# Kernel optimization log

Measured on AMD Instinct MI355X. Metric: run time of the kernel, lower is better.

## Reference

```python
import jax, jax.numpy as jnp
import numpy as np

H = 8        # n_attention_heads
D = 512      # model_dimension (full per-head dim in this module!)
DFF = 2048   # feed_forward_internal_dimension
B, T = 8, 1024
EPS = 1e-5


def _layernorm(x, g, b, eps=EPS):
    mu = jnp.mean(x, axis=-1, keepdims=True)
    var = jnp.mean(jnp.square(x - mu), axis=-1, keepdims=True)
    return (x - mu) * jax.lax.rsqrt(var + eps) * g + b


def setup_inputs() -> dict:
    key = jax.random.key(0)
    ks = jax.random.split(key, 16)
    s_d = 1.0 / np.sqrt(D)
    s_c = 1.0 / np.sqrt(H * D)
    s_f = 1.0 / np.sqrt(DFF)
    return {
        "x":   jax.random.normal(ks[0], (B, T, D), jnp.float32),
        # per-head projections, stored (in, out); stacked over heads
        "Wq":  jax.random.normal(ks[1], (H, D, D), jnp.float32) * s_d,
        "bq":  jax.random.normal(ks[2], (H, D), jnp.float32) * 0.02,
        "Wk":  jax.random.normal(ks[3], (H, D, D), jnp.float32) * s_d,
        "bk":  jax.random.normal(ks[4], (H, D), jnp.float32) * 0.02,
        "Wv":  jax.random.normal(ks[5], (H, D, D), jnp.float32) * s_d,
        "bv":  jax.random.normal(ks[6], (H, D), jnp.float32) * 0.02,
        "Wo":  jax.random.normal(ks[7], (H * D, D), jnp.float32) * s_c,
        "bo":  jax.random.normal(ks[8], (D,), jnp.float32) * 0.02,
        "ln1_g": 1.0 + 0.1 * jax.random.normal(ks[9], (D,), jnp.float32),
        "ln1_b": 0.1 * jax.random.normal(ks[10], (D,), jnp.float32),
        "W1":  jax.random.normal(ks[11], (D, DFF), jnp.float32) * s_d,
        "b1":  jax.random.normal(ks[12], (DFF,), jnp.float32) * 0.02,
        "W2":  jax.random.normal(ks[13], (DFF, D), jnp.float32) * s_f,
        "b2":  jax.random.normal(ks[14], (D,), jnp.float32) * 0.02,
        "ln2_g": 1.0 + 0.1 * jax.random.normal(ks[15], (D,), jnp.float32),
        "ln2_b": jnp.zeros((D,), jnp.float32),
    }


def reference(x, Wq, bq, Wk, bk, Wv, bv, Wo, bo, ln1_g, ln1_b,
              W1, b1, W2, b2, ln2_g, ln2_b):
    # --- multi-head attention (each head uses the FULL d_model) ---
    # q,k,v: [H, B, T, D]
    q = jnp.einsum("btd,hde->hbte", x, Wq) + bq[:, None, None, :]
    k = jnp.einsum("btd,hde->hbte", x, Wk) + bk[:, None, None, :]
    v = jnp.einsum("btd,hde->hbte", x, Wv) + bv[:, None, None, :]
    scores = jnp.einsum("hbte,hbse->hbts", q, k) * (D ** -0.5)  # [H,B,T,T]
    attn = jax.nn.softmax(scores, axis=-1)
    heads = jnp.einsum("hbts,hbse->hbte", attn, v)  # [H,B,T,D]
    # concat heads along features: [B,T,H*D]
    concat = jnp.transpose(heads, (1, 2, 0, 3)).reshape(x.shape[0], x.shape[1], -1)
    mha = concat @ Wo + bo
    # residual + LayerNorm (dropout_p = 0)
    y1 = _layernorm(mha + x, ln1_g, ln1_b)
    # --- FFN: note source applies ReLU AFTER the second Linear, then skip ---
    ff = jax.nn.relu((y1 @ W1 + b1) @ W2 + b2) + y1
    out = _layernorm(ff, ln2_g, ln2_b)
    return out
```

## Files before the change

kernel.cpp:

```cpp
#include <hip/hip_runtime.h>

using u16 = unsigned short;
using bf16x8 = __attribute__((ext_vector_type(8))) short;
using f32x4 = __attribute__((ext_vector_type(4))) float;
using f32x16 = __attribute__((ext_vector_type(16))) float;

__device__ __forceinline__ u16 f2bf(float f) {
  unsigned x = __float_as_uint(f);
  x += 0x7fffu + ((x >> 16) & 1u);
  return (u16)(x >> 16);
}

__device__ __forceinline__ void gl2lds16(const u16* g, u16* l) {
  __builtin_amdgcn_global_load_lds(
      (const __attribute__((address_space(1))) unsigned int*)g,
      (__attribute__((address_space(3))) unsigned int*)l, 16, 0, 0);
}

__global__ __launch_bounds__(256) void cvt_all(
    const float* __restrict__ x, u16* __restrict__ Krep,
    const float* __restrict__ Wq, const float* __restrict__ Wk,
    const float* __restrict__ Wv, const float* __restrict__ Wo,
    const float* __restrict__ W1, const float* __restrict__ W2,
    u16* __restrict__ Wqb, u16* __restrict__ Wkb, u16* __restrict__ WvT,
    u16* __restrict__ WoT, u16* __restrict__ W1T, u16* __restrict__ W2T)
{
  int b = blockIdx.x, tid = threadIdx.x;
  if (b < 4096) {
    int i = b * 1024 + tid * 4;
    float4 v = *(const float4*)(x + i);
    ushort4 o;
    o.x = f2bf(v.x); o.y = f2bf(v.y); o.z = f2bf(v.z); o.w = f2bf(v.w);
    *(ushort4*)(Krep + i) = o;
    return;
  }
  if (b < 8192) {
    const float* s; u16* d; int i;
    if (b < 6144) { s = Wq; d = Wqb; i = (b - 4096) * 1024 + tid * 4; }
    else          { s = Wk; d = Wkb; i = (b - 6144) * 1024 + tid * 4; }
    float4 v = *(const float4*)(s + i);
    ushort4 o;
    o.x = f2bf(v.x); o.y = f2bf(v.y); o.z = f2bf(v.z); o.w = f2bf(v.w);
    *(ushort4*)(d + i) = o;
    return;
  }
  __shared__ float T[32][33];
  const float* s; u16* d; int K, N, k0, n0;
  int i = b - 8192;
  if (i < 2048) {
    int h = i / 256, tl = i % 256;
    s = Wv + (size_t)h * 262144; d = WvT + (size_t)h * 262144;
    K = 512; N = 512; n0 = (tl % 16) * 32; k0 = (tl / 16) * 32;
  } else if (i < 4096) {
    int j = i - 2048;
    s = Wo; d = WoT; K = 4096; N = 512; n0 = (j % 16) * 32; k0 = (j / 16) * 32;
  } else if (i < 5120) {
    int j = i - 4096;
    s = W1; d = W1T; K = 512; N = 2048; n0 = (j % 64) * 32; k0 = (j / 64) * 32;
  } else {
    int j = i - 5120;
    s = W2; d = W2T; K = 2048; N = 512; n0 = (j % 16) * 32; k0 = (j / 16) * 32;
  }
  int r = tid >> 3, c4 = (tid & 7) << 2;
  float4 v = *(const float4*)(s + (size_t)(k0 + r) * N + n0 + c4);
  T[r][c4 + 0] = v.x; T[r][c4 + 1] = v.y; T[r][c4 + 2] = v.z; T[r][c4 + 3] = v.w;
  __syncthreads();
  ushort4 o;
  o.x = f2bf(T[c4 + 0][r]); o.y = f2bf(T[c4 + 1][r]);
  o.z = f2bf(T[c4 + 2][r]); o.w = f2bf(T[c4 + 3][r]);
  *(ushort4*)(d + (size_t)(n0 + r) * K + k0 + c4) = o;
}

__global__ __launch_bounds__(256) void wk_bias(
    const float* __restrict__ Wk, const float* __restrict__ bq,
    float* __restrict__ wbuf)
{
  int r = blockIdx.x * 4 + (threadIdx.x >> 6);
  int lane = threadIdx.x & 63;
  int h = r >> 9, a = r & 511;
  const float* row = Wk + ((size_t)h * 512 + a) * 512 + lane * 8;
  const float* bqp = bq + h * 512 + lane * 8;
  float4 w0 = *(const float4*)row, w1 = *(const float4*)(row + 4);
  float4 b0 = *(const float4*)bqp, b1 = *(const float4*)(bqp + 4);
  float s = w0.x * b0.x + w0.y * b0.y + w0.z * b0.z + w0.w * b0.w +
            w1.x * b1.x + w1.y * b1.y + w1.z * b1.z + w1.w * b1.w;
  #pragma unroll
  for (int off = 1; off < 64; off <<= 1) s += __shfl_xor(s, off);
  if (lane == 0) wbuf[r] = s;
}

template<int BM>
__global__ __launch_bounds__(256) void gemm_bt(
    const u16* __restrict__ A, const u16* __restrict__ Bt,
    const float* __restrict__ bias, void* __restrict__ Cout,
    int M, int N, int K, int lda, int ldb, long long kzoff,
    long long sBz, long long sbz, long long sCzBytes, int out_mode)
{
  constexpr int MT = BM / 32;
  __shared__ __align__(16) u16 smem[BM * 32 + 128 * 32];
  u16* As = smem;
  u16* Bs = smem + BM * 32;
  const f32x4 zero4 = {0.f, 0.f, 0.f, 0.f};

  const u16* Ap = A + (size_t)blockIdx.z * (size_t)kzoff;
  const u16* Bp = Bt + (size_t)blockIdx.z * (size_t)(sBz + kzoff);
  const float* biasp = bias ? bias + (size_t)blockIdx.z * sbz : nullptr;
  char* Cp = (char*)Cout + (size_t)blockIdx.z * sCzBytes;

  int tid = threadIdx.x;
  int lane = tid & 63, wave = tid >> 6;
  int m = lane & 15, quad = lane >> 4;
  int wm = (wave >> 1) * (BM / 2), wn = (wave & 1) * 64;
  int m0 = blockIdx.y * BM, n0 = blockIdx.x * 128;
  int lr = lane >> 2, lc = (lane & 3) << 3;

  f32x4 acc[MT][4];
  #pragma unroll
  for (int i = 0; i < MT; i++)
    #pragma unroll
    for (int j = 0; j < 4; j++) acc[i][j] = zero4;

  for (int k0 = 0; k0 < K; k0 += 32) {
    #pragma unroll
    for (int i = 0; i < BM / 64; i++) {
      int rb = i * 64 + wave * 16;
      gl2lds16(Ap + (size_t)(m0 + rb + lr) * lda + k0 + lc, &As[rb * 32]);
    }
    #pragma unroll
    for (int i = 0; i < 2; i++) {
      int rb = i * 64 + wave * 16;
      gl2lds16(Bp + (size_t)(n0 + rb + lr) * ldb + k0 + lc, &Bs[rb * 32]);
    }
    __syncthreads();

    bf16x8 af[MT], bfr[4];
    #pragma unroll
    for (int t = 0; t < MT; t++)
      af[t] = *(const bf16x8*)&As[(wm + t * 16 + m) * 32 + quad * 8];
    #pragma unroll
    for (int t = 0; t < 4; t++)
      bfr[t] = *(const bf16x8*)&Bs[(wn + t * 16 + m) * 32 + quad * 8];
    #pragma unroll
    for (int mt = 0; mt < MT; mt++)
      #pragma unroll
      for (int nt = 0; nt < 4; nt++)
        acc[mt][nt] = __builtin_amdgcn_mfma_f32_16x16x32_bf16(af[mt], bfr[nt],
                                                              acc[mt][nt], 0, 0, 0);
    __syncthreads();
  }

  if (out_mode == 2) {
    u16* Ts = smem;
    int b2 = m0 >> 10, t20 = m0 & 1023;
    int half = wave >> 1;
    #pragma unroll
    for (int mt = 0; mt < MT; mt++) {
      #pragma unroll
      for (int nt = 0; nt < 4; nt++) {
        int colc = wn + nt * 16 + m;
        float bb = biasp ? biasp[n0 + colc] : 0.f;
        #pragma unroll
        for (int r = 0; r < 4; r++)
          Ts[colc * 40 + half * 16 + quad * 4 + r] = f2bf(acc[mt][nt][r] + bb);
      }
      __syncthreads();
      #pragma unroll
      for (int it = 0; it < 2; it++) {
        int c = (tid >> 2) + 64 * it;
        int j = tid & 3;
        bf16x8 v = *(const bf16x8*)&Ts[c * 40 + j * 8];
        int tg = t20 + (j >> 1) * (BM / 2) + mt * 16 + (j & 1) * 8;
        *(bf16x8*)((u16*)Cp + ((size_t)b2 * 512 + n0 + c) * 1024 + tg) = v;
      }
      __syncthreads();
    }
    return;
  }

  #pragma unroll
  for (int nt = 0; nt < 4; nt++) {
    int col = n0 + wn + nt * 16 + m;
    float bb = biasp ? biasp[col] : 0.f;
    #pragma unroll
    for (int mt = 0; mt < MT; mt++) {
      #pragma unroll
      for (int r = 0; r < 4; r++) {
        int row = m0 + wm + mt * 16 + quad * 4 + r;
        float v = acc[mt][nt][r] + bb;
        if (out_mode == 1) {
          ((u16*)Cp)[(size_t)row * N + col] = f2bf(v);
        } else {
          ((float*)Cp)[(size_t)row * N + col] = v;
        }
      }
    }
  }
}

__global__ __launch_bounds__(256) void gemm_tv16(
    const u16* __restrict__ A, const u16* __restrict__ Mt,
    const u16* __restrict__ WvT, const float* __restrict__ wbuf,
    const float* __restrict__ bv, u16* __restrict__ Tg, u16* __restrict__ Vg)
{
  __shared__ __align__(16) u16 smem[8192];
  u16* As = smem;
  u16* Bs = smem + 4096;
  const f32x4 zero4 = {0.f, 0.f, 0.f, 0.f};

  int z = blockIdx.z;
  int t = z >> 3, h = z & 7;
  const u16* Bp = (t == 0 ? Mt : WvT) + (size_t)h * 262144;
  const float* biasp = (t == 0 ? wbuf : bv) + h * 512;
  u16* Og = (t == 0 ? Tg : Vg) + (size_t)h * 4194304;

  int tid = threadIdx.x;
  int lane = tid & 63, wave = tid >> 6;
  int m = lane & 15, quad = lane >> 4;
  int wm = (wave >> 1) * 64, wn = (wave & 1) * 64;
  int m0 = blockIdx.y * 128, n0 = blockIdx.x * 128;
  int lr = lane >> 2, lc = (lane & 3) << 3;

  f32x4 acc[4][4];
  #pragma unroll
  for (int i = 0; i < 4; i++)
    #pragma unroll
    for (int j = 0; j < 4; j++) acc[i][j] = zero4;

  for (int k0 = 0; k0 < 512; k0 += 32) {
    #pragma unroll
    for (int i = 0; i < 2; i++) {
      int rb = i * 64 + wave * 16;
      gl2lds16(A + (size_t)(m0 + rb + lr) * 512 + k0 + lc, &As[rb * 32]);
      gl2lds16(Bp + (size_t)(n0 + rb + lr) * 512 + k0 + lc, &Bs[rb * 32]);
    }
    __syncthreads();
    bf16x8 af[4], bfr[4];
    #pragma unroll
    for (int tt = 0; tt < 4; tt++) {
      af[tt]  = *(const bf16x8*)&As[(wm + tt * 16 + m) * 32 + quad * 8];
      bfr[tt] = *(const bf16x8*)&Bs[(wn + tt * 16 + m) * 32 + quad * 8];
    }
    #pragma unroll
    for (int mt = 0; mt < 4; mt++)
      #pragma unroll
      for (int nt = 0; nt < 4; nt++)
        acc[mt][nt] = __builtin_amdgcn_mfma_f32_16x16x32_bf16(af[mt], bfr[nt],
                                                              acc[mt][nt], 0, 0, 0);
    __syncthreads();
  }

  if (t == 1) {
    u16* Ts = smem;
    int b2 = m0 >> 10, t20 = m0 & 1023;
    int half = wave >> 1;
    #pragma unroll
    for (int mt = 0; mt < 4; mt++) {
      #pragma unroll
      for (int nt = 0; nt < 4; nt++) {
        int colc = wn + nt * 16 + m;
        float bb = biasp[n0 + colc];
        #pragma unroll
        for (int r = 0; r < 4; r++)
          Ts[colc * 40 + half * 16 + quad * 4 + r] = f2bf(acc[mt][nt][r] + bb);
      }
      __syncthreads();
      #pragma unroll
      for (int it = 0; it < 2; it++) {
        int c = (tid >> 2) + 64 * it;
        int j = tid & 3;
        bf16x8 v = *(const bf16x8*)&Ts[c * 40 + j * 8];
        int tg = t20 + (j >> 1) * 64 + mt * 16 + (j & 1) * 8;
        *(bf16x8*)(Og + ((size_t)b2 * 512 + n0 + c) * 1024 + tg) = v;
      }
      __syncthreads();
    }
    return;
  }

  #pragma unroll
  for (int nt = 0; nt < 4; nt++) {
    int col = n0 + wn + nt * 16 + m;
    float bb = biasp[col];
    #pragma unroll
    for (int mt = 0; mt < 4; mt++) {
      #pragma unroll
      for (int r = 0; r < 4; r++) {
        int row = m0 + wm + mt * 16 + quad * 4 + r;
        Og[(size_t)row * 512 + col] = f2bf(acc[mt][nt][r] + bb);
      }
    }
  }
}

__global__ __launch_bounds__(256, 2) void attn_kernel(
    const u16* __restrict__ Tg, const u16* __restrict__ Krep,
    const u16* __restrict__ Vg, u16* __restrict__ Oc, int h0)
{
  __shared__ __align__(16) u16 Kt[32][520];
  __shared__ __align__(16) u16 Vt[512 * 32];
  __shared__ __align__(16) u16 Pl[64][40];
  __shared__ float lred[64];
  const f32x4 zero4 = {0.f, 0.f, 0.f, 0.f};
  const f32x16 zero16 = {0.f,0.f,0.f,0.f,0.f,0.f,0.f,0.f,
                         0.f,0.f,0.f,0.f,0.f,0.f,0.f,0.f};

  int b = blockIdx.x, qb = blockIdx.y, z = blockIdx.z;
  int h = h0 + z;

  size_t hb = ((size_t)z * 8 + b) * (size_t)(1024 * 512);
  const u16* Tp = Tg + hb;
  const u16* Kp = Krep + (size_t)b * (size_t)(1024 * 512);
  const u16* Vp = Vg + hb;

  int tid = threadIdx.x, lane = tid & 63, wave = tid >> 6;
  int m = lane & 15, quad = lane >> 4;
  int l31 = lane & 31, hi = lane >> 5;
  int qh = wave >> 1, dh = wave & 1;
  int q0 = qb * 64 + wave * 16;

  int vr = lane >> 2;
  int vc = (((lane & 3) ^ ((lane >> 3) & 3)) << 3);
  int vswz = (l31 >> 1) & 3;

  bf16x8 aq[16];
  #pragma unroll
  for (int kc = 0; kc < 16; kc++)
    aq[kc] = *(const bf16x8*)(Tp + (size_t)(q0 + m) * 512 + kc * 32 + quad * 8);

  f32x16 o[8];
  #pragma unroll
  for (int dt = 0; dt < 8; dt++) o[dt] = zero16;
  float lsum_acc[4] = {0.f, 0.f, 0.f, 0.f};
  const float scale = 0.04419417382415922f;

  #pragma unroll
  for (int r = 0; r < 8; r++) {
    int row = wave * 8 + r;
    gl2lds16(Kp + (size_t)row * 512 + lane * 8, &Kt[row][0]);
  }
  #pragma unroll
  for (int j = 0; j < 8; j++) {
    int rb = wave * 128 + j * 16;
    gl2lds16(Vp + (size_t)(rb + vr) * 1024 + vc, &Vt[rb * 32]);
  }

  for (int kt = 0; kt < 32; kt++) {
    asm volatile("s_waitcnt vmcnt(8)" ::: "memory");
    __builtin_amdgcn_sched_barrier(0);
    __builtin_amdgcn_s_barrier();
    __builtin_amdgcn_sched_barrier(0);

    f32x4 s0 = zero4, s1 = zero4;
    #pragma unroll
    for (int kc = 0; kc < 16; kc++) {
      bf16x8 bk0 = *(const bf16x8*)&Kt[m][kc * 32 + quad * 8];
      bf16x8 bk1 = *(const bf16x8*)&Kt[m + 16][kc * 32 + quad * 8];
      s0 = __builtin_amdgcn_mfma_f32_16x16x32_bf16(aq[kc], bk0, s0, 0, 0, 0);
      s1 = __builtin_amdgcn_mfma_f32_16x16x32_bf16(aq[kc], bk1, s1, 0, 0, 0);
    }

    #pragma unroll
    for (int r = 0; r < 4; r++) {
      float e0 = __expf(s0[r] * scale);
      float e1 = __expf(s1[r] * scale);
      u16 p0 = f2bf(e0), p1 = f2bf(e1);
      int prow = wave * 16 + quad * 4 + r;
      Pl[prow][m] = p0;
      Pl[prow][m + 16] = p1;
      float t = __uint_as_float((unsigned)p0 << 16) +
                __uint_as_float((unsigned)p1 << 16);
      t += __shfl_xor(t, 1); t += __shfl_xor(t, 2);
      t += __shfl_xor(t, 4); t += __shfl_xor(t, 8);
      lsum_acc[r] += t;
    }

    asm volatile("s_waitcnt vmcnt(0) lgkmcnt(0)" ::: "memory");
    __builtin_amdgcn_sched_barrier(0);
    __builtin_amdgcn_s_barrier();
    __builtin_amdgcn_sched_barrier(0);

    if (kt < 31) {
      int kr1 = (kt + 1) * 32;
      #pragma unroll
      for (int r = 0; r < 8; r++) {
        int row = wave * 8 + r;
        gl2lds16(Kp + (size_t)(kr1 + row) * 512 + lane * 8, &Kt[row][0]);
      }
    }

    const u16* PlRow = &Pl[qh * 32 + l31][0];
    #pragma unroll
    for (int ks = 0; ks < 2; ks++) {
      bf16x8 pa = *(const bf16x8*)(PlRow + ks * 16 + hi * 8);
      #pragma unroll
      for (int dt = 0; dt < 8; dt++) {
        int rr = dh * 256 + dt * 32 + l31;
        int cc2 = (((ks * 2 + hi) ^ vswz) << 3);
        bf16x8 bv = *(const bf16x8*)&Vt[rr * 32 + cc2];
        o[dt] = __builtin_amdgcn_mfma_f32_32x32x16_bf16(pa, bv, o[dt], 0, 0, 0);
      }
    }

    asm volatile("s_waitcnt lgkmcnt(0)" ::: "memory");
    __builtin_amdgcn_sched_barrier(0);
    __builtin_amdgcn_s_barrier();
    __builtin_amdgcn_sched_barrier(0);

    if (kt < 31) {
      int kr1 = (kt + 1) * 32;
      #pragma unroll
      for (int j = 0; j < 8; j++) {
        int rb = wave * 128 + j * 16;
        gl2lds16(Vp + (size_t)(rb + vr) * 1024 + kr1 + vc, &Vt[rb * 32]);
      }
    }
  }

  if (m == 0) {
    #pragma unroll
    for (int r = 0; r < 4; r++)
      lred[wave * 16 + quad * 4 + r] = lsum_acc[r];
  }
  __syncthreads();

  float linv[16];
  #pragma unroll
  for (int g = 0; g < 4; g++) {
    float4 t = *(const float4*)&lred[qh * 32 + 8 * g + 4 * hi];
    linv[4 * g + 0] = 1.f / t.x; linv[4 * g + 1] = 1.f / t.y;
    linv[4 * g + 2] = 1.f / t.z; linv[4 * g + 3] = 1.f / t.w;
  }

  size_t obase = (size_t)b * 1024 + qb * 64 + qh * 32;
  #pragma unroll
  for (int dt = 0; dt < 8; dt++) {
    int dcol = dh * 256 + dt * 32 + l31;
    #pragma unroll
    for (int reg = 0; reg < 16; reg++) {
      int rowq = (reg & 3) + 8 * (reg >> 2) + 4 * hi;
      Oc[((obase + rowq) * 8 + h) * 512 + dcol] = f2bf(o[dt][reg] * linv[reg]);
    }
  }
}

__global__ __launch_bounds__(256) void ln_kernel(
    const float* __restrict__ xin0, const float* __restrict__ xin1,
    const float* __restrict__ bias, const float* __restrict__ res,
    const float* __restrict__ gam, const float* __restrict__ bet,
    float* __restrict__ outf, u16* __restrict__ outb, int do_relu)
{
  __shared__ float red[4];
  __shared__ float red2[4];
  int row = blockIdx.x, t = threadIdx.x;
  size_t base = (size_t)row * 512;
  float a0 = xin0[base + t] + bias[t];
  float a1 = xin0[base + 256 + t] + bias[256 + t];
  if (xin1) { a0 += xin1[base + t]; a1 += xin1[base + 256 + t]; }
  if (do_relu) { a0 = fmaxf(a0, 0.f); a1 = fmaxf(a1, 0.f); }
  a0 += res[base + t]; a1 += res[base + 256 + t];

  float s = a0 + a1;
  #pragma unroll
  for (int off = 32; off > 0; off >>= 1) s += __shfl_xor(s, off);
  if ((t & 63) == 0) red[t >> 6] = s;
  __syncthreads();
  float mu = (red[0] + red[1] + red[2] + red[3]) * (1.f / 512.f);

  float d0 = a0 - mu, d1 = a1 - mu;
  float q = d0 * d0 + d1 * d1;
  #pragma unroll
  for (int off = 32; off > 0; off >>= 1) q += __shfl_xor(q, off);
  if ((t & 63) == 0) red2[t >> 6] = q;
  __syncthreads();
  float var = (red2[0] + red2[1] + red2[2] + red2[3]) * (1.f / 512.f);
  float rs = rsqrtf(var + 1e-5f);

  float o0 = d0 * rs * gam[t] + bet[t];
  float o1 = d1 * rs * gam[t + 256] + bet[t + 256];
  outf[base + t] = o0;
  outf[base + 256 + t] = o1;
  if (outb) { outb[base + t] = f2bf(o0); outb[base + 256 + t] = f2bf(o1); }
}

extern "C" void kernel_launch(void* const* d_in, const int* in_sizes, int n_in,
                              void* d_out, int out_size, void* d_ws, size_t ws_size,
                              hipStream_t stream) {
  const float* x   = (const float*)d_in[0];
  const float* Wq  = (const float*)d_in[1];
  const float* bq  = (const float*)d_in[2];
  const float* Wk  = (const float*)d_in[3];
  const float* bk  = (const float*)d_in[4];
  const float* Wv  = (const float*)d_in[5];
  const float* bv  = (const float*)d_in[6];
  const float* Wo  = (const float*)d_in[7];
  const float* bo  = (const float*)d_in[8];
  const float* g1  = (const float*)d_in[9];
  const float* bn1 = (const float*)d_in[10];
  const float* W1  = (const float*)d_in[11];
  const float* bf1 = (const float*)d_in[12];
  const float* W2  = (const float*)d_in[13];
  const float* bf2 = (const float*)d_in[14];
  const float* g2  = (const float*)d_in[15];
  const float* bn2 = (const float*)d_in[16];
  (void)bk;

  const size_t HB = 8388608;
  char* ws = (char*)d_ws;
  u16* Krep = (u16*)(ws + 0);
  u16* xb   = Krep;
  u16* Wqb = (u16*)(ws + 67108864);
  u16* Wkb = (u16*)(ws + 71303168);
  u16* WvT = (u16*)(ws + 75497472);
  u16* WoT = (u16*)(ws + 79691776);
  u16* W1T = (u16*)(ws + 83886080);
  u16* W2T = (u16*)(ws + 85983232);
  u16* Mt  = (u16*)(ws + 88080384);
  float* wbuf = (float*)(ws + 92274688);
  u16* cc  = (u16*)(ws + 92291072);
  size_t tvbase = 159399936;
  size_t G = 1;
  if (ws_size >= 293617664ULL) G = 8;
  else if (ws_size >= 226508800ULL) G = 4;
  else if (ws_size >= 218120192ULL) G = 2;
  u16* Tg = (u16*)(ws + tvbase);
  u16* Vg = (u16*)(ws + tvbase + G * HB);
  float* y1f  = (float*)(ws + 159399936);
  u16*   y1b  = (u16*)(ws + 176177152);
  float* mha0 = (float*)(ws + 184565760);
  float* mha1 = (float*)(ws + 201342976);
  u16*   ff1  = (u16*)(ws + 92291072);
  float* ff20 = (float*)(ws + 125845504);
  float* ff21 = (float*)(ws + 142622720);

  cvt_all<<<14336, 256, 0, stream>>>(x, Krep, Wq, Wk, Wv, Wo, W1, W2,
                                     Wqb, Wkb, WvT, WoT, W1T, W2T);
  gemm_bt<128><<<dim3(4, 4, 8), 256, 0, stream>>>(Wkb, Wqb, nullptr, Mt,
      512, 512, 512, 512, 512, 262144LL, 0LL, 0LL, 524288LL, 1);
  wk_bias<<<1024, 256, 0, stream>>>(Wk, bq, wbuf);

  dim3 blk(256);
  if (G == 8) {
    gemm_tv16<<<dim3(4, 64, 16), blk, 0, stream>>>(xb, Mt, WvT, wbuf, bv,
                                                   Tg, Vg);
    attn_kernel<<<dim3(8, 16, 8), 256, 0, stream>>>(Tg, Krep, Vg, cc, 0);
  } else {
    for (int h0 = 0; h0 < 8; h0 += (int)G) {
      dim3 gqkv(4, 64, (unsigned)G);
      gemm_bt<128><<<gqkv, blk, 0, stream>>>(xb, Mt + (size_t)h0 * 262144,
          wbuf + h0 * 512, Tg, 8192, 512, 512, 512, 512, 0LL,
          262144LL, 512LL, (long long)HB, 1);
      gemm_bt<128><<<gqkv, blk, 0, stream>>>(xb, WvT + (size_t)h0 * 262144,
          bv + h0 * 512, Vg, 8192, 512, 512, 512, 512, 0LL,
          262144LL, 512LL, (long long)HB, 2);
      attn_kernel<<<dim3(8, 16, (unsigned)G), 256, 0, stream>>>(Tg, Krep, Vg,
                                                                cc, h0);
    }
  }

  gemm_bt<64><<<dim3(4, 128, 2), blk, 0, stream>>>(cc, WoT, nullptr, mha0,
      8192, 512, 2048, 4096, 4096, 2048LL, 0LL, 0LL, 16777216LL, 0);
  ln_kernel<<<8192, 256, 0, stream>>>(mha0, mha1, bo, x, g1, bn1, y1f, y1b, 0);

  gemm_bt<128><<<dim3(16, 64, 1), blk, 0, stream>>>(y1b, W1T, bf1, ff1,
      8192, 2048, 512, 512, 512, 0LL, 0LL, 0LL, 0LL, 1);

  gemm_bt<64><<<dim3(4, 128, 2), blk, 0, stream>>>(ff1, W2T, nullptr, ff20,
      8192, 512, 1024, 2048, 2048, 1024LL, 0LL, 0LL, 16777216LL, 0);

  ln_kernel<<<8192, 256, 0, stream>>>(ff20, ff21, bf2, y1f, g2, bn2,
                                      (float*)d_out, nullptr, 1);
}
```

Baseline: 661.5 us.

## Fold Wv into Wo and attend over transposed x instead of V

Attention now multiplies the softmax weights directly by a transposed bf16 copy of x, so the per-head V projection is no longer computed. Wv is instead folded into the output projection through a precomputed Wv·Wo product per head, and bv·Wo is folded into the output bias, since softmax rows sum to one. This removes the V GEMM and the large Vg write and read, adding only a small weight-by-weight GEMM and an x transpose. The softmax row-sum shuffle reduction is also moved out of the inner loop to run once at the end. Rounding the combined Wv·Wo weight to bf16 changes numerics slightly.

Result: faster. 570.8 us (-13.7%).

```diff
diff --git a/kernel.cpp b/kernel.cpp
--- a/kernel.cpp
+++ b/kernel.cpp
@@ -18,26 +18,20 @@
 }
 
 __global__ __launch_bounds__(256) void cvt_all(
-    const float* __restrict__ x, u16* __restrict__ Krep,
+    const float* __restrict__ x, u16* __restrict__ Krep, u16* __restrict__ XT,
     const float* __restrict__ Wq, const float* __restrict__ Wk,
     const float* __restrict__ Wv, const float* __restrict__ Wo,
     const float* __restrict__ W1, const float* __restrict__ W2,
-    u16* __restrict__ Wqb, u16* __restrict__ Wkb, u16* __restrict__ WvT,
+    u16* __restrict__ Wqb, u16* __restrict__ Wkb, u16* __restrict__ Wvb,
     u16* __restrict__ WoT, u16* __restrict__ W1T, u16* __restrict__ W2T)
 {
   int b = blockIdx.x, tid = threadIdx.x;
-  if (b < 4096) {
-    int i = b * 1024 + tid * 4;
-    float4 v = *(const float4*)(x + i);
-    ushort4 o;
-    o.x = f2bf(v.x); o.y = f2bf(v.y); o.z = f2bf(v.z); o.w = f2bf(v.w);
-    *(ushort4*)(Krep + i) = o;
-    return;
-  }
-  if (b < 8192) {
+  if (b < 10240) {
     const float* s; u16* d; int i;
-    if (b < 6144) { s = Wq; d = Wqb; i = (b - 4096) * 1024 + tid * 4; }
-    else          { s = Wk; d = Wkb; i = (b - 6144) * 1024 + tid * 4; }
+    if (b < 4096)      { s = x;  d = Krep; i = b * 1024 + tid * 4; }
+    else if (b < 6144) { s = Wq; d = Wqb;  i = (b - 4096) * 1024 + tid * 4; }
+    else if (b < 8192) { s = Wk; d = Wkb;  i = (b - 6144) * 1024 + tid * 4; }
+    else               { s = Wv; d = Wvb;  i = (b - 8192) * 1024 + tid * 4; }
     float4 v = *(const float4*)(s + i);
     ushort4 o;
     o.x = f2bf(v.x); o.y = f2bf(v.y); o.z = f2bf(v.z); o.w = f2bf(v.w);
@@ -46,19 +40,19 @@
   }
   __shared__ float T[32][33];
   const float* s; u16* d; int K, N, k0, n0;
-  int i = b - 8192;
-  if (i < 2048) {
-    int h = i / 256, tl = i % 256;
-    s = Wv + (size_t)h * 262144; d = WvT + (size_t)h * 262144;
-    K = 512; N = 512; n0 = (tl % 16) * 32; k0 = (tl / 16) * 32;
-  } else if (i < 4096) {
-    int j = i - 2048;
+  int i = b - 10240;
+  if (i < 4096) {
+    int b8 = i >> 9, j = i & 511;
+    s = x + (size_t)b8 * 524288; d = XT + (size_t)b8 * 524288;
+    K = 1024; N = 512; n0 = (j % 16) * 32; k0 = (j / 16) * 32;
+  } else if (i < 6144) {
+    int j = i - 4096;
     s = Wo; d = WoT; K = 4096; N = 512; n0 = (j % 16) * 32; k0 = (j / 16) * 32;
-  } else if (i < 5120) {
-    int j = i - 4096;
+  } else if (i < 7168) {
+    int j = i - 6144;
     s = W1; d = W1T; K = 512; N = 2048; n0 = (j % 64) * 32; k0 = (j / 64) * 32;
   } else {
-    int j = i - 5120;
+    int j = i - 7168;
     s = W2; d = W2T; K = 2048; N = 512; n0 = (j % 16) * 32; k0 = (j / 16) * 32;
   }
   int r = tid >> 3, c4 = (tid & 7) << 2;
@@ -89,6 +83,26 @@
   if (lane == 0) wbuf[r] = s;
 }
 
+__global__ __launch_bounds__(256) void bo_fold(
+    const float* __restrict__ bv, const float* __restrict__ Wo,
+    const float* __restrict__ bo, float* __restrict__ bop)
+{
+  __shared__ float part[16][17];
+  int ei = threadIdx.x & 15, ch = threadIdx.x >> 4;
+  int e = blockIdx.x * 16 + ei;
+  float s = 0.f;
+  for (int k = ch * 256; k < ch * 256 + 256; k++)
+    s += bv[k] * Wo[(size_t)k * 512 + e];
+  part[ei][ch] = s;
+  __syncthreads();
+  if (threadIdx.x < 16) {
+    float t = bo[blockIdx.x * 16 + threadIdx.x];
+    #pragma unroll
+    for (int c = 0; c < 16; c++) t += part[threadIdx.x][c];
+    bop[blockIdx.x * 16 + threadIdx.x] = t;
+  }
+}
+
 template<int BM>
 __global__ __launch_bounds__(256) void gemm_bt(
     const u16* __restrict__ A, const u16* __restrict__ Bt,
@@ -197,21 +211,19 @@
   }
 }
 
-__global__ __launch_bounds__(256) void gemm_tv16(
+__global__ __launch_bounds__(256) void gemm_t8(
     const u16* __restrict__ A, const u16* __restrict__ Mt,
-    const u16* __restrict__ WvT, const float* __restrict__ wbuf,
-    const float* __restrict__ bv, u16* __restrict__ Tg, u16* __restrict__ Vg)
+    const float* __restrict__ wbuf, u16* __restrict__ Tg)
 {
   __shared__ __align__(16) u16 smem[8192];
   u16* As = smem;
   u16* Bs = smem + 4096;
   const f32x4 zero4 = {0.f, 0.f, 0.f, 0.f};
 
-  int z = blockIdx.z;
-  int t = z >> 3, h = z & 7;
-  const u16* Bp = (t == 0 ? Mt : WvT) + (size_t)h * 262144;
-  const float* biasp = (t == 0 ? wbuf : bv) + h * 512;
-  u16* Og = (t == 0 ? Tg : Vg) + (size_t)h * 4194304;
+  int h = blockIdx.z;
+  const u16* Bp = Mt + (size_t)h * 262144;
+  const float* biasp = wbuf + h * 512;
+  u16* Og = Tg + (size_t)h * 4194304;
 
   int tid = threadIdx.x;
   int lane = tid & 63, wave = tid >> 6;
@@ -249,34 +261,6 @@
     __syncthreads();
   }
 
-  if (t == 1) {
-    u16* Ts = smem;
-    int b2 = m0 >> 10, t20 = m0 & 1023;
-    int half = wave >> 1;
-    #pragma unroll
-    for (int mt = 0; mt < 4; mt++) {
-      #pragma unroll
-      for (int nt = 0; nt < 4; nt++) {
-        int colc = wn + nt * 16 + m;
-        float bb = biasp[n0 + colc];
-        #pragma unroll
-        for (int r = 0; r < 4; r++)
-          Ts[colc * 40 + half * 16 + quad * 4 + r] = f2bf(acc[mt][nt][r] + bb);
-      }
-      __syncthreads();
-      #pragma unroll
-      for (int it = 0; it < 2; it++) {
-        int c = (tid >> 2) + 64 * it;
-        int j = tid & 3;
-        bf16x8 v = *(const bf16x8*)&Ts[c * 40 + j * 8];
-        int tg = t20 + (j >> 1) * 64 + mt * 16 + (j & 1) * 8;
-        *(bf16x8*)(Og + ((size_t)b2 * 512 + n0 + c) * 1024 + tg) = v;
-      }
-      __syncthreads();
-    }
-    return;
-  }
-
   #pragma unroll
   for (int nt = 0; nt < 4; nt++) {
     int col = n0 + wn + nt * 16 + m;
@@ -294,7 +278,7 @@
 
 __global__ __launch_bounds__(256, 2) void attn_kernel(
     const u16* __restrict__ Tg, const u16* __restrict__ Krep,
-    const u16* __restrict__ Vg, u16* __restrict__ Oc, int h0)
+    const u16* __restrict__ XT, u16* __restrict__ Oc, int h0)
 {
   __shared__ __align__(16) u16 Kt[32][520];
   __shared__ __align__(16) u16 Vt[512 * 32];
@@ -310,7 +294,7 @@
   size_t hb = ((size_t)z * 8 + b) * (size_t)(1024 * 512);
   const u16* Tp = Tg + hb;
   const u16* Kp = Krep + (size_t)b * (size_t)(1024 * 512);
-  const u16* Vp = Vg + hb;
+  const u16* Vp = XT + (size_t)b * (size_t)(512 * 1024);
 
   int tid = threadIdx.x, lane = tid & 63, wave = tid >> 6;
   int m = lane & 15, quad = lane >> 4;
@@ -367,11 +351,8 @@
       int prow = wave * 16 + quad * 4 + r;
       Pl[prow][m] = p0;
       Pl[prow][m + 16] = p1;
-      float t = __uint_as_float((unsigned)p0 << 16) +
-                __uint_as_float((unsigned)p1 << 16);
-      t += __shfl_xor(t, 1); t += __shfl_xor(t, 2);
-      t += __shfl_xor(t, 4); t += __shfl_xor(t, 8);
-      lsum_acc[r] += t;
+      lsum_acc[r] += __uint_as_float((unsigned)p0 << 16) +
+                     __uint_as_float((unsigned)p1 << 16);
     }
 
     asm volatile("s_waitcnt vmcnt(0) lgkmcnt(0)" ::: "memory");
@@ -416,6 +397,13 @@
     }
   }
 
+  #pragma unroll
+  for (int r = 0; r < 4; r++) {
+    float t = lsum_acc[r];
+    t += __shfl_xor(t, 1); t += __shfl_xor(t, 2);
+    t += __shfl_xor(t, 4); t += __shfl_xor(t, 8);
+    lsum_acc[r] = t;
+  }
   if (m == 0) {
     #pragma unroll
     for (int r = 0; r < 4; r++)
@@ -504,26 +492,22 @@
   const float* bn2 = (const float*)d_in[16];
   (void)bk;
 
-  const size_t HB = 8388608;
   char* ws = (char*)d_ws;
   u16* Krep = (u16*)(ws + 0);
   u16* xb   = Krep;
   u16* Wqb = (u16*)(ws + 67108864);
   u16* Wkb = (u16*)(ws + 71303168);
-  u16* WvT = (u16*)(ws + 75497472);
+  u16* Wvb = (u16*)(ws + 75497472);
   u16* WoT = (u16*)(ws + 79691776);
   u16* W1T = (u16*)(ws + 83886080);
   u16* W2T = (u16*)(ws + 85983232);
   u16* Mt  = (u16*)(ws + 88080384);
   float* wbuf = (float*)(ws + 92274688);
   u16* cc  = (u16*)(ws + 92291072);
-  size_t tvbase = 159399936;
-  size_t G = 1;
-  if (ws_size >= 293617664ULL) G = 8;
-  else if (ws_size >= 226508800ULL) G = 4;
-  else if (ws_size >= 218120192ULL) G = 2;
-  u16* Tg = (u16*)(ws + tvbase);
-  u16* Vg = (u16*)(ws + tvbase + G * HB);
+  u16* Tg  = (u16*)(ws + 159399936);
+  u16* XT  = (u16*)(ws + 226508800);
+  u16* WvWoT = (u16*)(ws + 234897408);
+  float* bop = (float*)(ws + 239091712);
   float* y1f  = (float*)(ws + 159399936);
   u16*   y1b  = (u16*)(ws + 176177152);
   float* mha0 = (float*)(ws + 184565760);
@@ -532,39 +516,26 @@
   float* ff20 = (float*)(ws + 125845504);
   float* ff21 = (float*)(ws + 142622720);
 
-  cvt_all<<<14336, 256, 0, stream>>>(x, Krep, Wq, Wk, Wv, Wo, W1, W2,
-                                     Wqb, Wkb, WvT, WoT, W1T, W2T);
+  bo_fold<<<32, 256, 0, stream>>>(bv, Wo, bo, bop);
+  cvt_all<<<18432, 256, 0, stream>>>(x, Krep, XT, Wq, Wk, Wv, Wo, W1, W2,
+                                     Wqb, Wkb, Wvb, WoT, W1T, W2T);
   gemm_bt<128><<<dim3(4, 4, 8), 256, 0, stream>>>(Wkb, Wqb, nullptr, Mt,
       512, 512, 512, 512, 512, 262144LL, 0LL, 0LL, 524288LL, 1);
   wk_bias<<<1024, 256, 0, stream>>>(Wk, bq, wbuf);
-
-  dim3 blk(256);
-  if (G == 8) {
-    gemm_tv16<<<dim3(4, 64, 16), blk, 0, stream>>>(xb, Mt, WvT, wbuf, bv,
-                                                   Tg, Vg);
-    attn_kernel<<<dim3(8, 16, 8), 256, 0, stream>>>(Tg, Krep, Vg, cc, 0);
-  } else {
-    for (int h0 = 0; h0 < 8; h0 += (int)G) {
-      dim3 gqkv(4, 64, (unsigned)G);
-      gemm_bt<128><<<gqkv, blk, 0, stream>>>(xb, Mt + (size_t)h0 * 262144,
-          wbuf + h0 * 512, Tg, 8192, 512, 512, 512, 512, 0LL,
-          262144LL, 512LL, (long long)HB, 1);
-      gemm_bt<128><<<gqkv, blk, 0, stream>>>(xb, WvT + (size_t)h0 * 262144,
-          bv + h0 * 512, Vg, 8192, 512, 512, 512, 512, 0LL,
-          262144LL, 512LL, (long long)HB, 2);
-      attn_kernel<<<dim3(8, 16, (unsigned)G), 256, 0, stream>>>(Tg, Krep, Vg,
-                                                                cc, h0);
-    }
-  }
-
-  gemm_bt<64><<<dim3(4, 128, 2), blk, 0, stream>>>(cc, WoT, nullptr, mha0,
+  gemm_bt<128><<<dim3(4, 4, 8), 256, 0, stream>>>(WoT, Wvb, nullptr, WvWoT,
+      512, 4096, 512, 4096, 512, 512LL, 261632LL, 0LL, 1024LL, 1);
+
+  gemm_t8<<<dim3(4, 64, 8), 256, 0, stream>>>(xb, Mt, wbuf, Tg);
+  attn_kernel<<<dim3(8, 16, 8), 256, 0, stream>>>(Tg, Krep, XT, cc, 0);
+
+  gemm_bt<64><<<dim3(4, 128, 2), 256, 0, stream>>>(cc, WvWoT, nullptr, mha0,
       8192, 512, 2048, 4096, 4096, 2048LL, 0LL, 0LL, 16777216LL, 0);
-  ln_kernel<<<8192, 256, 0, stream>>>(mha0, mha1, bo, x, g1, bn1, y1f, y1b, 0);
-
-  gemm_bt<128><<<dim3(16, 64, 1), blk, 0, stream>>>(y1b, W1T, bf1, ff1,
+  ln_kernel<<<8192, 256, 0, stream>>>(mha0, mha1, bop, x, g1, bn1, y1f, y1b, 0);
+
+  gemm_bt<128><<<dim3(16, 64, 1), 256, 0, stream>>>(y1b, W1T, bf1, ff1,
       8192, 2048, 512, 512, 512, 0LL, 0LL, 0LL, 0LL, 1);
 
-  gemm_bt<64><<<dim3(4, 128, 2), blk, 0, stream>>>(ff1, W2T, nullptr, ff20,
+  gemm_bt<64><<<dim3(4, 128, 2), 256, 0, stream>>>(ff1, W2T, nullptr, ff20,
       8192, 512, 1024, 2048, 2048, 1024LL, 0LL, 0LL, 16777216LL, 0);
 
   ln_kernel<<<8192, 256, 0, stream>>>(ff20, ff21, bf2, y1f, g2, bn2,
```
